# Kernel tuning notes

Measured on AMD Instinct MI355X. Metric: run time of the kernel, lower is better.

## Reference

```python
import jax, jax.numpy as jnp
import numpy as np

N_NODES = 100000
N_EDGES = 1600000
IN_DIM = 128
OUT_DIM = 64


def setup_inputs() -> dict:
    key = jax.random.key(0)
    k1, k2, k3, k4, k5, k6 = jax.random.split(key, 6)
    x = jax.random.normal(k1, (N_NODES, IN_DIM), dtype=jnp.float32)
    edge_row = jax.random.randint(k2, (N_EDGES,), 0, N_NODES, dtype=jnp.int32)
    edge_col = jax.random.randint(k3, (N_EDGES,), 0, N_NODES, dtype=jnp.int32)
    edge_val = jax.random.uniform(k4, (N_EDGES,), dtype=jnp.float32)
    W = jax.random.normal(k5, (IN_DIM, OUT_DIM), dtype=jnp.float32) * (1.0 / np.sqrt(IN_DIM))
    b = jax.random.normal(k6, (OUT_DIM,), dtype=jnp.float32) * 0.01
    return {"x": x, "edge_row": edge_row, "edge_col": edge_col,
            "edge_val": edge_val, "W": W, "b": b}


def reference(x, edge_row, edge_col, edge_val, W, b):
    # xw = Linear(x)  -> [N, OUT_DIM]
    xw = x @ W + b
    # SpMM: (A_hat @ xw)[r] = sum_e val[e] * xw[col[e]] for edges with row[e]==r
    msgs = edge_val[:, None] * xw[edge_col]          # [E, OUT_DIM]
    ax = jax.ops.segment_sum(msgs, edge_row, num_segments=N_NODES)  # [N, OUT_DIM]
    # ReLU; dropout p=0.0 is identity (eval mode)
    return jax.nn.relu(ax)
```

## Files before the change

### kernel.cpp

```cpp
#include <hip/hip_runtime.h>
#include <hip/hip_fp16.h>
#include <limits.h>

#define IN_DIM 128
#define OUT_DIM 64
#define NBUCK 782
#define RPB 128
#define CHUNK 4096
#define SCAP 4096


typedef _Float16 half8_t __attribute__((ext_vector_type(8)));
typedef float    f32x4  __attribute__((ext_vector_type(4)));

__device__ __forceinline__ int kmap(int g, int j) {
    return g * 4 + (j & 3) + 16 * (j >> 2);
}

__global__ __launch_bounds__(256) void prep_kernel(
    const float* __restrict__ W, __half* __restrict__ wf,
    int* __restrict__ bcount, int* __restrict__ cursor,
    int* __restrict__ row_ptr, int n_nodes, int n_edges) {
    const int t = threadIdx.x;
    for (int idx = t; idx < 4 * 4 * 64 * 8; idx += 256) {
        const int j    = idx & 7;
        const int lane = (idx >> 3) & 63;
        const int ks   = (idx >> 9) & 3;
        const int n    = idx >> 11;
        const int col  = n * 16 + (lane & 15);
        const int k    = ks * 32 + kmap(lane >> 4, j);
        wf[idx] = __float2half(W[k * OUT_DIM + col]);
    }
    if (bcount)
        for (int i = t; i < NBUCK; i += 256) { bcount[i] = 0; cursor[i] = 0; }
    if (row_ptr && t == 0) row_ptr[n_nodes] = n_edges;
}

__global__ __launch_bounds__(256) void gemm_hist_kernel(
    const float* __restrict__ x, const __half* __restrict__ wf,
    const float* __restrict__ b, __half* __restrict__ xw, int n_nodes,
    const int* __restrict__ erow, int* __restrict__ bcount, int n_edges) {
    __shared__ int h[NBUCK];
    const int t  = threadIdx.x;
    const int l  = t & 63;
    const int wv = t >> 6;
    const int g  = l >> 4;
    const int rowbase = blockIdx.x * 64 + wv * 16;
    const int row = rowbase + (l & 15);
    const bool rok = row < n_nodes;
    const float* xr = x + (size_t)row * IN_DIM;

    half8_t bf[4][4];
    const half8_t* wf8 = (const half8_t*)wf;
    #pragma unroll
    for (int n = 0; n < 4; ++n)
        #pragma unroll
        for (int ks = 0; ks < 4; ++ks)
            bf[n][ks] = wf8[(n * 4 + ks) * 64 + l];

    half8_t af[4];
    #pragma unroll
    for (int ks = 0; ks < 4; ++ks) {
        float4 c0 = rok ? *(const float4*)(xr + ks * 32 + g * 4)
                        : make_float4(0.f, 0.f, 0.f, 0.f);
        float4 c1 = rok ? *(const float4*)(xr + ks * 32 + 16 + g * 4)
                        : make_float4(0.f, 0.f, 0.f, 0.f);
        half8_t a;
        a[0] = (_Float16)c0.x; a[1] = (_Float16)c0.y;
        a[2] = (_Float16)c0.z; a[3] = (_Float16)c0.w;
        a[4] = (_Float16)c1.x; a[5] = (_Float16)c1.y;
        a[6] = (_Float16)c1.z; a[7] = (_Float16)c1.w;
        af[ks] = a;
    }

    f32x4 acc[4];
    #pragma unroll
    for (int n = 0; n < 4; ++n) acc[n] = (f32x4){0.f, 0.f, 0.f, 0.f};

    #pragma unroll
    for (int ks = 0; ks < 4; ++ks)
        #pragma unroll
        for (int n = 0; n < 4; ++n)
            acc[n] = __builtin_amdgcn_mfma_f32_16x16x32_f16(af[ks], bf[n][ks], acc[n], 0, 0, 0);

    float bias[4];
    #pragma unroll
    for (int n = 0; n < 4; ++n) bias[n] = b[n * 16 + (l & 15)];

    #pragma unroll
    for (int n = 0; n < 4; ++n)
        #pragma unroll
        for (int q = 0; q < 4; ++q) {
            const int ro = rowbase + g * 4 + q;
            if (ro < n_nodes)
                xw[(size_t)ro * OUT_DIM + n * 16 + (l & 15)] =
                    __float2half(acc[n][q] + bias[n]);
        }

    if (bcount && blockIdx.x < 512) {
        for (int i = t; i < NBUCK; i += 256) h[i] = 0;
        __syncthreads();
        const int stride = 512 * 256;
        for (int e = blockIdx.x * 256 + t; e < n_edges; e += stride)
            atomicAdd(&h[erow[e] >> 7], 1);
        __syncthreads();
        for (int i = t; i < NBUCK; i += 256)
            if (h[i]) atomicAdd(&bcount[i], h[i]);
    }
}

__global__ __launch_bounds__(512) void partition_kernel(
    const int* __restrict__ erow, const int* __restrict__ ecol,
    const float* __restrict__ eval_, const int* __restrict__ bcount,
    int* __restrict__ cursor, int2* __restrict__ ecs, int n_edges) {
    __shared__ int  hist[NBUCK];
    __shared__ int  lbase[NBUCK];
    __shared__ int  gdelta[NBUCK];
    __shared__ int  sbase[NBUCK];
    __shared__ int2 data[CHUNK];
    __shared__ int  gpos[CHUNK];
    __shared__ int  wsum[8];

    const int t = threadIdx.x;
    const int base = blockIdx.x * CHUNK;
    const int cnt = min(CHUNK, n_edges - base);

    for (int i = t; i < NBUCK; i += 512) hist[i] = 0;

    {
        const int i0 = 2 * t, i1 = 2 * t + 1;
        const int v0 = (i0 < NBUCK) ? bcount[i0] : 0;
        const int v1 = (i1 < NBUCK) ? bcount[i1] : 0;
        const int s2 = v0 + v1;
        int inc = s2;
        #pragma unroll
        for (int d = 1; d < 64; d <<= 1) {
            int u = __shfl_up(inc, d, 64);
            if ((t & 63) >= d) inc += u;
        }
        if ((t & 63) == 63) wsum[t >> 6] = inc;
        __syncthreads();
        int wp = 0;
        #pragma unroll
        for (int w = 0; w < 8; ++w) if (w < (t >> 6)) wp += wsum[w];
        const int ex = wp + (inc - s2);
        if (i0 < NBUCK) sbase[i0] = ex;
        if (i1 < NBUCK) sbase[i1] = ex + v0;
    }

    int   myrow[CHUNK / 512];
    int   mycol[CHUNK / 512];
    float myval[CHUNK / 512];
    #pragma unroll
    for (int i = 0; i < CHUNK / 512; ++i) {
        const int idx = t + i * 512;
        if (idx < cnt) {
            const int e = base + idx;
            myrow[i] = erow[e];
            mycol[i] = ecol[e];
            myval[i] = eval_[e];
            atomicAdd(&hist[myrow[i] >> 7], 1);
        }
    }
    __syncthreads();

    {
        const int i0 = 2 * t, i1 = 2 * t + 1;
        const int v0 = (i0 < NBUCK) ? hist[i0] : 0;
        const int v1 = (i1 < NBUCK) ? hist[i1] : 0;
        const int s2 = v0 + v1;
        int inc = s2;
        #pragma unroll
        for (int d = 1; d < 64; d <<= 1) {
            int u = __shfl_up(inc, d, 64);
            if ((t & 63) >= d) inc += u;
        }
        if ((t & 63) == 63) wsum[t >> 6] = inc;
        __syncthreads();
        int wp = 0;
        #pragma unroll
        for (int w = 0; w < 8; ++w) if (w < (t >> 6)) wp += wsum[w];
        const int ex = wp + (inc - s2);
        if (i0 < NBUCK) lbase[i0] = ex;
        if (i1 < NBUCK) lbase[i1] = ex + v0;
    }
    __syncthreads();

    for (int i = t; i < NBUCK; i += 512) {
        const int c = hist[i];
        gdelta[i] = c ? (sbase[i] + atomicAdd(&cursor[i], c) - lbase[i]) : 0;
    }
    __syncthreads();

    #pragma unroll
    for (int i = 0; i < CHUNK / 512; ++i) {
        const int idx = t + i * 512;
        if (idx < cnt) {
            const int bk = myrow[i] >> 7;
            const int slot = atomicAdd(&lbase[bk], 1);
            int2 p;
            p.x = (int)(((unsigned)(myrow[i] & (RPB - 1)) << 25) |
                        ((unsigned)mycol[i] << 7));
            p.y = __float_as_int(myval[i]);
            data[slot] = p;
            gpos[slot] = slot + gdelta[bk];
        }
    }
    __syncthreads();

    for (int slot = t; slot < cnt; slot += 512)
        ecs[gpos[slot]] = data[slot];
}

__global__ __launch_bounds__(512) void sort_kernel(
    const int* __restrict__ bcount, int2* __restrict__ ecs,
    int* __restrict__ row_ptr, int* __restrict__ bbase, int n_nodes) {
    __shared__ int2 data[SCAP];
    __shared__ int2 data2[SCAP];
    __shared__ int  hist[RPB];
    __shared__ int  sbase[NBUCK + 1];
    __shared__ int  wsum[8];
    __shared__ int  wtot;

    const int bk = blockIdx.x;
    const int t  = threadIdx.x;

    if (t < RPB) hist[t] = 0;

    {
        const int i0 = 2 * t, i1 = 2 * t + 1;
        const int v0 = (i0 < NBUCK) ? bcount[i0] : 0;
        const int v1 = (i1 < NBUCK) ? bcount[i1] : 0;
        const int s2 = v0 + v1;
        int inc = s2;
        #pragma unroll
        for (int d = 1; d < 64; d <<= 1) {
            int u = __shfl_up(inc, d, 64);
            if ((t & 63) >= d) inc += u;
        }
        if ((t & 63) == 63) wsum[t >> 6] = inc;
        __syncthreads();
        int wp = 0;
        #pragma unroll
        for (int w = 0; w < 8; ++w) if (w < (t >> 6)) wp += wsum[w];
        const int ex = wp + (inc - s2);
        if (i0 < NBUCK) sbase[i0] = ex;
        if (i1 < NBUCK) sbase[i1] = ex + v0;
        if (t == 511) sbase[NBUCK] = wp + inc;
    }
    __syncthreads();

    const int s   = sbase[bk];
    const int e   = sbase[bk + 1];
    const int cnt = e - s;
    const int rbase = bk * RPB;

    if (t == 0) {
        bbase[bk] = s;
        if (bk == NBUCK - 1) bbase[bk + 1] = e;
    }

    if (cnt > SCAP) {
        for (int r = t; r < RPB; r += 512)
            if (rbase + r < n_nodes) row_ptr[rbase + r] = INT_MIN;
        return;
    }

    for (int i = t; i < cnt; i += 512) {
        const int2 p = ecs[s + i];
        data[i] = p;
        atomicAdd(&hist[((unsigned)p.x) >> 25], 1);
    }
    __syncthreads();

    int inc = 0, v = 0;
    if (t < RPB) {
        v = hist[t];
        inc = v;
        #pragma unroll
        for (int d = 1; d < 64; d <<= 1) {
            int u = __shfl_up(inc, d, 64);
            if ((t & 63) >= d) inc += u;
        }
        if (t == 63) wtot = inc;
    }
    __syncthreads();
    if (t < RPB) {
        if (t >= 64) inc += wtot;
        const int ex = inc - v;
        if (rbase + t < n_nodes) row_ptr[rbase + t] = s + ex;
        hist[t] = ex;
    }
    __syncthreads();

    for (int i = t; i < cnt; i += 512) {
        const int2 p = data[i];
        const int pos = atomicAdd(&hist[((unsigned)p.x) >> 25], 1);
        data2[pos] = p;
    }
    __syncthreads();

    for (int i = t; i < cnt; i += 512) ecs[s + i] = data2[i];
}

__global__ __launch_bounds__(256) void gather_relu_kernel(
    const __half* __restrict__ xw, const int2* __restrict__ ecs,
    const int* __restrict__ row_ptr, const int* __restrict__ bbase,
    float* __restrict__ out, int n_nodes, int n_edges) {
    const int lane = threadIdx.x & 63;
    const int q    = lane & 7;
    const int g    = lane >> 3;
    const int wid  = (blockIdx.x * blockDim.x + threadIdx.x) >> 6;
    const int r0   = wid * 2;
    const int r1   = r0 + 1;
    if (r0 >= n_nodes) return;
    const bool has1 = (r1 < n_nodes);
    const char* xwb = (const char*)xw;

    const int s0raw = row_ptr[r0];
    const int s1raw = has1 ? row_ptr[r1] : INT_MIN;
    const bool ok0 = (s0raw != INT_MIN);
    const bool ok1 = has1 && (s1raw != INT_MIN);

    float acc0[8], acc1[8];
    #pragma unroll
    for (int i = 0; i < 8; ++i) { acc0[i] = 0.f; acc1[i] = 0.f; }

    if (ok0 && (ok1 || !has1)) {
        int e0;
        {
            const int n0 = row_ptr[r0 + 1];
            e0 = (n0 == INT_MIN) ? bbase[(r0 >> 7) + 1] : n0;
        }
        int e1 = 0, j1 = 0;
        if (ok1) {
            const int n1 = row_ptr[r1 + 1];
            e1 = (n1 == INT_MIN) ? bbase[(r1 >> 7) + 1] : n1;
            j1 = s1raw;
        }
        int j0 = s0raw;

        while (j0 < e0 || j1 < e1) {
            const bool a0 = j0 < e0;
            const bool a1 = j1 < e1;
            int2 p0, p1; float v0 = 0.f, v1 = 0.f;
            unsigned off0 = 0, off1 = 0;
            if (a0) {
                const int ei = j0 + g;
                p0 = ecs[min(ei, n_edges - 1)];
                v0 = (ei < e0) ? __int_as_float(p0.y) : 0.f;
                off0 = (((unsigned)p0.x) & 0x01FFFF80u) | ((unsigned)q << 4);
            }
            if (a1) {
                const int ei = j1 + g;
                p1 = ecs[min(ei, n_edges - 1)];
                v1 = (ei < e1) ? __int_as_float(p1.y) : 0.f;
                off1 = (((unsigned)p1.x) & 0x01FFFF80u) | ((unsigned)q << 4);
            }
            union { uint4 u; __half2 h[4]; } U0, U1;
            if (a0) U0.u = *(const uint4*)(xwb + off0);
            if (a1) U1.u = *(const uint4*)(xwb + off1);
            if (a0) {
                #pragma unroll
                for (int i = 0; i < 4; ++i) {
                    const float2 f = __half22float2(U0.h[i]);
                    acc0[2 * i]     = fmaf(v0, f.x, acc0[2 * i]);
                    acc0[2 * i + 1] = fmaf(v0, f.y, acc0[2 * i + 1]);
                }
                j0 += 8;
            }
            if (a1) {
                #pragma unroll
                for (int i = 0; i < 4; ++i) {
                    const float2 f = __half22float2(U1.h[i]);
                    acc1[2 * i]     = fmaf(v1, f.x, acc1[2 * i]);
                    acc1[2 * i + 1] = fmaf(v1, f.y, acc1[2 * i + 1]);
                }
                j1 += 8;
            }
        }
    } else {
        #pragma unroll 1
        for (int rr = 0; rr < 2; ++rr) {
            const int r = r0 + rr;
            if (r >= n_nodes) break;
            float* acc = rr ? acc1 : acc0;
            const int sr = row_ptr[r];
            if (sr != INT_MIN) {
                const int nr = row_ptr[r + 1];
                const int er = (nr == INT_MIN) ? bbase[(r >> 7) + 1] : nr;
                for (int j = sr; j < er; j += 8) {
                    const int ei = j + g;
                    const int2 p = ecs[min(ei, n_edges - 1)];
                    const float v = (ei < er) ? __int_as_float(p.y) : 0.f;
                    const unsigned off = (((unsigned)p.x) & 0x01FFFF80u) | ((unsigned)q << 4);
                    union { uint4 u; __half2 h[4]; } U;
                    U.u = *(const uint4*)(xwb + off);
                    #pragma unroll
                    for (int i = 0; i < 4; ++i) {
                        const float2 f = __half22float2(U.h[i]);
                        acc[2 * i]     = fmaf(v, f.x, acc[2 * i]);
                        acc[2 * i + 1] = fmaf(v, f.y, acc[2 * i + 1]);
                    }
                }
            } else {
                const int bk = r >> 7;
                const int bs = bbase[bk], be = bbase[bk + 1];
                const unsigned rl = (unsigned)(r & (RPB - 1));
                for (int j = bs; j < be; ++j) {
                    const int2 p = ecs[j];
                    if ((((unsigned)p.x) >> 25) == rl) {
                        const float v = __int_as_float(p.y);
                        const unsigned off = (((unsigned)p.x) & 0x01FFFF80u) | ((unsigned)q << 4);
                        union { uint4 u; __half2 h[4]; } U;
                        U.u = *(const uint4*)(xwb + off);
                        #pragma unroll
                        for (int i = 0; i < 4; ++i) {
                            const float2 f = __half22float2(U.h[i]);
                            acc[2 * i]     = fmaf(v * 0.125f, f.x, acc[2 * i]);
                            acc[2 * i + 1] = fmaf(v * 0.125f, f.y, acc[2 * i + 1]);
                        }
                    }
                }
            }
        }
    }

    #pragma unroll
    for (int d = 8; d < 64; d <<= 1) {
        #pragma unroll
        for (int i = 0; i < 8; ++i) {
            acc0[i] += __shfl_xor(acc0[i], d, 64);
            acc1[i] += __shfl_xor(acc1[i], d, 64);
        }
    }

    if (g == 0) {
        {
            float4 o0, o1;
            o0.x = fmaxf(acc0[0], 0.f); o0.y = fmaxf(acc0[1], 0.f);
            o0.z = fmaxf(acc0[2], 0.f); o0.w = fmaxf(acc0[3], 0.f);
            o1.x = fmaxf(acc0[4], 0.f); o1.y = fmaxf(acc0[5], 0.f);
            o1.z = fmaxf(acc0[6], 0.f); o1.w = fmaxf(acc0[7], 0.f);
            float* op = out + (size_t)r0 * OUT_DIM + q * 8;
            *(float4*)(op)     = o0;
            *(float4*)(op + 4) = o1;
        }
        if (has1) {
            float4 o0, o1;
            o0.x = fmaxf(acc1[0], 0.f); o0.y = fmaxf(acc1[1], 0.f);
            o0.z = fmaxf(acc1[2], 0.f); o0.w = fmaxf(acc1[3], 0.f);
            o1.x = fmaxf(acc1[4], 0.f); o1.y = fmaxf(acc1[5], 0.f);
            o1.z = fmaxf(acc1[6], 0.f); o1.w = fmaxf(acc1[7], 0.f);
            float* op = out + (size_t)r1 * OUT_DIM + q * 8;
            *(float4*)(op)     = o0;
            *(float4*)(op + 4) = o1;
        }
    }
}

__global__ __launch_bounds__(256) void edge_scatter_kernel(
    const __half* __restrict__ xw, const int* __restrict__ erow,
    const int* __restrict__ ecol, const float* __restrict__ eval_,
    float* __restrict__ out, int n_edges) {
    const int lane  = threadIdx.x & 63;
    const int wid   = (blockIdx.x * blockDim.x + threadIdx.x) >> 6;
    const int nwave = (gridDim.x * blockDim.x) >> 6;
    for (int e = wid; e < n_edges; e += nwave) {
        const float m = eval_[e] * __half2float(xw[(size_t)ecol[e] * OUT_DIM + lane]);
        atomicAdd(&out[(size_t)erow[e] * OUT_DIM + lane], m);
    }
}

__global__ __launch_bounds__(256) void relu_kernel(float4* __restrict__ p, int n4) {
    const int stride = gridDim.x * blockDim.x;
    for (int i = blockIdx.x * blockDim.x + threadIdx.x; i < n4; i += stride) {
        float4 v = p[i];
        v.x = fmaxf(v.x, 0.f); v.y = fmaxf(v.y, 0.f);
        v.z = fmaxf(v.z, 0.f); v.w = fmaxf(v.w, 0.f);
        p[i] = v;
    }
}

extern "C" void kernel_launch(void* const* d_in, const int* in_sizes, int n_in,
                              void* d_out, int out_size, void* d_ws, size_t ws_size,
                              hipStream_t stream) {
    const float* x     = (const float*)d_in[0];
    const int*   erow  = (const int*)d_in[1];
    const int*   ecol  = (const int*)d_in[2];
    const float* eval_ = (const float*)d_in[3];
    const float* W     = (const float*)d_in[4];
    const float* b     = (const float*)d_in[5];
    float*       out   = (float*)d_out;

    const int n_nodes = in_sizes[0] / IN_DIM;
    const int n_edges = in_sizes[1];

    auto align256 = [](size_t v) { return (v + 255) & ~(size_t)255; };
    size_t off_xw     = 0;
    size_t off_wf     = align256(off_xw     + (size_t)n_nodes * OUT_DIM * 2);
    size_t off_bcount = align256(off_wf     + (size_t)4 * 4 * 64 * 8 * 2);
    size_t off_cursor = align256(off_bcount + (size_t)NBUCK * 4);
    size_t off_bbase  = align256(off_cursor + (size_t)NBUCK * 4);
    size_t off_rowptr = align256(off_bbase  + (size_t)(NBUCK + 1) * 4);
    size_t off_ecs    = align256(off_rowptr + (size_t)(n_nodes + 1) * 4);
    size_t need       = off_ecs + (size_t)n_edges * 8;

    __half* xw = (__half*)((char*)d_ws + off_xw);
    __half* wf = (__half*)((char*)d_ws + off_wf);

    const bool main_path = (need <= ws_size) && (n_nodes <= NBUCK * RPB) && (n_edges > 0);

    if (main_path) {
        int*  bcount = (int*)((char*)d_ws + off_bcount);
        int*  cursor = (int*)((char*)d_ws + off_cursor);
        int*  bbase  = (int*)((char*)d_ws + off_bbase);
        int*  rowptr = (int*)((char*)d_ws + off_rowptr);
        int2* ecs    = (int2*)((char*)d_ws + off_ecs);

        prep_kernel<<<1, 256, 0, stream>>>(W, wf, bcount, cursor, rowptr, n_nodes, n_edges);
        gemm_hist_kernel<<<(n_nodes + 63) / 64, 256, 0, stream>>>(
            x, wf, b, xw, n_nodes, erow, bcount, n_edges);
        partition_kernel<<<(n_edges + CHUNK - 1) / CHUNK, 512, 0, stream>>>(
            erow, ecol, eval_, bcount, cursor, ecs, n_edges);
        sort_kernel<<<NBUCK, 512, 0, stream>>>(bcount, ecs, rowptr, bbase, n_nodes);
        gather_relu_kernel<<<(n_nodes + 7) / 8, 256, 0, stream>>>(
            xw, ecs, rowptr, bbase, out, n_nodes, n_edges);
    } else {
        prep_kernel<<<1, 256, 0, stream>>>(W, wf, nullptr, nullptr, nullptr, n_nodes, n_edges);
        gemm_hist_kernel<<<(n_nodes + 63) / 64, 256, 0, stream>>>(
            x, wf, b, xw, n_nodes, nullptr, nullptr, 0);
        hipMemsetAsync(d_out, 0, (size_t)out_size * sizeof(float), stream);
        edge_scatter_kernel<<<8192, 256, 0, stream>>>(xw, erow, ecol, eval_, out, n_edges);
        relu_kernel<<<2048, 256, 0, stream>>>((float4*)d_out, out_size / 4);
    }
}
```

Measured before the change: 112.3 us.

## Fuse per-bucket sort and gather-ReLU into one kernel using shared memory

```diff
diff --git a/kernel.cpp b/kernel.cpp
--- a/kernel.cpp
+++ b/kernel.cpp
@@ -19,8 +19,7 @@
 
 __global__ __launch_bounds__(256) void prep_kernel(
     const float* __restrict__ W, __half* __restrict__ wf,
-    int* __restrict__ bcount, int* __restrict__ cursor,
-    int* __restrict__ row_ptr, int n_nodes, int n_edges) {
+    int* __restrict__ bcount, int* __restrict__ cursor) {
     const int t = threadIdx.x;
     for (int idx = t; idx < 4 * 4 * 64 * 8; idx += 256) {
         const int j    = idx & 7;
@@ -33,7 +32,6 @@
     }
     if (bcount)
         for (int i = t; i < NBUCK; i += 256) { bcount[i] = 0; cursor[i] = 0; }
-    if (row_ptr && t == 0) row_ptr[n_nodes] = n_edges;
 }
 
 __global__ __launch_bounds__(256) void gemm_hist_kernel(
@@ -212,18 +210,23 @@
         ecs[gpos[slot]] = data[slot];
 }
 
-__global__ __launch_bounds__(512) void sort_kernel(
-    const int* __restrict__ bcount, int2* __restrict__ ecs,
-    int* __restrict__ row_ptr, int* __restrict__ bbase, int n_nodes) {
+__global__ __launch_bounds__(512) void bucket_gather_kernel(
+    const __half* __restrict__ xw, const int2* __restrict__ ecs,
+    const int* __restrict__ bcount, float* __restrict__ out,
+    int n_nodes, int n_edges) {
     __shared__ int2 data[SCAP];
-    __shared__ int2 data2[SCAP];
     __shared__ int  hist[RPB];
+    __shared__ int  rstart[RPB + 1];
     __shared__ int  sbase[NBUCK + 1];
     __shared__ int  wsum[8];
     __shared__ int  wtot;
 
-    const int bk = blockIdx.x;
-    const int t  = threadIdx.x;
+    const int bk   = blockIdx.x;
+    const int t    = threadIdx.x;
+    const int lane = t & 63;
+    const int wv   = t >> 6;
+    const int q    = lane & 7;
+    const int g    = lane >> 3;
 
     if (t < RPB) hist[t] = 0;
 
@@ -250,149 +253,144 @@
     }
     __syncthreads();
 
-    const int s   = sbase[bk];
-    const int e   = sbase[bk + 1];
-    const int cnt = e - s;
+    const int s     = sbase[bk];
+    const int e     = sbase[bk + 1];
+    const int cnt   = e - s;
     const int rbase = bk * RPB;
-
-    if (t == 0) {
-        bbase[bk] = s;
-        if (bk == NBUCK - 1) bbase[bk + 1] = e;
-    }
-
-    if (cnt > SCAP) {
-        for (int r = t; r < RPB; r += 512)
-            if (rbase + r < n_nodes) row_ptr[rbase + r] = INT_MIN;
-        return;
-    }
-
-    for (int i = t; i < cnt; i += 512) {
-        const int2 p = ecs[s + i];
-        data[i] = p;
-        atomicAdd(&hist[((unsigned)p.x) >> 25], 1);
-    }
-    __syncthreads();
-
-    int inc = 0, v = 0;
-    if (t < RPB) {
-        v = hist[t];
-        inc = v;
-        #pragma unroll
-        for (int d = 1; d < 64; d <<= 1) {
-            int u = __shfl_up(inc, d, 64);
-            if ((t & 63) >= d) inc += u;
-        }
-        if (t == 63) wtot = inc;
-    }
-    __syncthreads();
-    if (t < RPB) {
-        if (t >= 64) inc += wtot;
-        const int ex = inc - v;
-        if (rbase + t < n_nodes) row_ptr[rbase + t] = s + ex;
-        hist[t] = ex;
-    }
-    __syncthreads();
-
-    for (int i = t; i < cnt; i += 512) {
-        const int2 p = data[i];
-        const int pos = atomicAdd(&hist[((unsigned)p.x) >> 25], 1);
-        data2[pos] = p;
-    }
-    __syncthreads();
-
-    for (int i = t; i < cnt; i += 512) ecs[s + i] = data2[i];
-}
-
-__global__ __launch_bounds__(256) void gather_relu_kernel(
-    const __half* __restrict__ xw, const int2* __restrict__ ecs,
-    const int* __restrict__ row_ptr, const int* __restrict__ bbase,
-    float* __restrict__ out, int n_nodes, int n_edges) {
-    const int lane = threadIdx.x & 63;
-    const int q    = lane & 7;
-    const int g    = lane >> 3;
-    const int wid  = (blockIdx.x * blockDim.x + threadIdx.x) >> 6;
-    const int r0   = wid * 2;
-    const int r1   = r0 + 1;
-    if (r0 >= n_nodes) return;
-    const bool has1 = (r1 < n_nodes);
     const char* xwb = (const char*)xw;
 
-    const int s0raw = row_ptr[r0];
-    const int s1raw = has1 ? row_ptr[r1] : INT_MIN;
-    const bool ok0 = (s0raw != INT_MIN);
-    const bool ok1 = has1 && (s1raw != INT_MIN);
-
-    float acc0[8], acc1[8];
-    #pragma unroll
-    for (int i = 0; i < 8; ++i) { acc0[i] = 0.f; acc1[i] = 0.f; }
-
-    if (ok0 && (ok1 || !has1)) {
-        int e0;
+    if (cnt <= SCAP) {
+        for (int i = t; i < cnt; i += 512)
+            atomicAdd(&hist[((unsigned)ecs[s + i].x) >> 25], 1);
+        __syncthreads();
+
         {
-            const int n0 = row_ptr[r0 + 1];
-            e0 = (n0 == INT_MIN) ? bbase[(r0 >> 7) + 1] : n0;
-        }
-        int e1 = 0, j1 = 0;
-        if (ok1) {
-            const int n1 = row_ptr[r1 + 1];
-            e1 = (n1 == INT_MIN) ? bbase[(r1 >> 7) + 1] : n1;
-            j1 = s1raw;
-        }
-        int j0 = s0raw;
-
-        while (j0 < e0 || j1 < e1) {
-            const bool a0 = j0 < e0;
-            const bool a1 = j1 < e1;
-            int2 p0, p1; float v0 = 0.f, v1 = 0.f;
-            unsigned off0 = 0, off1 = 0;
-            if (a0) {
-                const int ei = j0 + g;
-                p0 = ecs[min(ei, n_edges - 1)];
-                v0 = (ei < e0) ? __int_as_float(p0.y) : 0.f;
-                off0 = (((unsigned)p0.x) & 0x01FFFF80u) | ((unsigned)q << 4);
-            }
-            if (a1) {
-                const int ei = j1 + g;
-                p1 = ecs[min(ei, n_edges - 1)];
-                v1 = (ei < e1) ? __int_as_float(p1.y) : 0.f;
-                off1 = (((unsigned)p1.x) & 0x01FFFF80u) | ((unsigned)q << 4);
-            }
-            union { uint4 u; __half2 h[4]; } U0, U1;
-            if (a0) U0.u = *(const uint4*)(xwb + off0);
-            if (a1) U1.u = *(const uint4*)(xwb + off1);
-            if (a0) {
+            int inc = 0, v = 0;
+            if (t < RPB) {
+                v = hist[t];
+                inc = v;
                 #pragma unroll
-                for (int i = 0; i < 4; ++i) {
-                    const float2 f = __half22float2(U0.h[i]);
-                    acc0[2 * i]     = fmaf(v0, f.x, acc0[2 * i]);
-                    acc0[2 * i + 1] = fmaf(v0, f.y, acc0[2 * i + 1]);
-                }
-                j0 += 8;
-            }
-            if (a1) {
+                for (int d = 1; d < 64; d <<= 1) {
+                    int u = __shfl_up(inc, d, 64);
+                    if ((t & 63) >= d) inc += u;
+                }
+                if (t == 63) wtot = inc;
+            }
+            __syncthreads();
+            if (t < RPB) {
+                if (t >= 64) inc += wtot;
+                rstart[t] = inc - v;
+                hist[t]   = inc - v;
+                if (t == RPB - 1) rstart[RPB] = inc;
+            }
+        }
+        __syncthreads();
+
+        for (int i = t; i < cnt; i += 512) {
+            const int2 p = ecs[s + i];
+            const int pos = atomicAdd(&hist[((unsigned)p.x) >> 25], 1);
+            data[pos] = p;
+        }
+        __syncthreads();
+
+        for (int rp = 0; rp < 8; ++rp) {
+            const int rl0 = wv * 16 + rp * 2;
+            const int rl1 = rl0 + 1;
+            int j0 = rstart[rl0];
+            const int e0 = rstart[rl0 + 1];
+            int j1 = rstart[rl1];
+            const int e1 = rstart[rl1 + 1];
+
+            float acc0[8], acc1[8];
+            #pragma unroll
+            for (int i = 0; i < 8; ++i) { acc0[i] = 0.f; acc1[i] = 0.f; }
+
+            while (j0 < e0 || j1 < e1) {
+                const bool a0 = j0 < e0;
+                const bool a1 = j1 < e1;
+                float v0 = 0.f, v1 = 0.f;
+                unsigned off0 = 0, off1 = 0;
+                if (a0) {
+                    const int ei = j0 + g;
+                    const int2 p = data[min(ei, cnt - 1)];
+                    v0 = (ei < e0) ? __int_as_float(p.y) : 0.f;
+                    off0 = (((unsigned)p.x) & 0x01FFFF80u) | ((unsigned)q << 4);
+                }
+                if (a1) {
+                    const int ei = j1 + g;
+                    const int2 p = data[min(ei, cnt - 1)];
+                    v1 = (ei < e1) ? __int_as_float(p.y) : 0.f;
+                    off1 = (((unsigned)p.x) & 0x01FFFF80u) | ((unsigned)q << 4);
+                }
+                union { uint4 u; __half2 h[4]; } U0, U1;
+                if (a0) U0.u = *(const uint4*)(xwb + off0);
+                if (a1) U1.u = *(const uint4*)(xwb + off1);
+                if (a0) {
+                    #pragma unroll
+                    for (int i = 0; i < 4; ++i) {
+                        const float2 f = __half22float2(U0.h[i]);
+                        acc0[2 * i]     = fmaf(v0, f.x, acc0[2 * i]);
+                        acc0[2 * i + 1] = fmaf(v0, f.y, acc0[2 * i + 1]);
+                    }
+                    j0 += 8;
+                }
+                if (a1) {
+                    #pragma unroll
+                    for (int i = 0; i < 4; ++i) {
+                        const float2 f = __half22float2(U1.h[i]);
+                        acc1[2 * i]     = fmaf(v1, f.x, acc1[2 * i]);
+                        acc1[2 * i + 1] = fmaf(v1, f.y, acc1[2 * i + 1]);
+                    }
+                    j1 += 8;
+                }
+            }
+
+            #pragma unroll
+            for (int d = 8; d < 64; d <<= 1) {
                 #pragma unroll
-                for (int i = 0; i < 4; ++i) {
-                    const float2 f = __half22float2(U1.h[i]);
-                    acc1[2 * i]     = fmaf(v1, f.x, acc1[2 * i]);
-                    acc1[2 * i + 1] = fmaf(v1, f.y, acc1[2 * i + 1]);
-                }
-                j1 += 8;
+                for (int i = 0; i < 8; ++i) {
+                    acc0[i] += __shfl_xor(acc0[i], d, 64);
+                    acc1[i] += __shfl_xor(acc1[i], d, 64);
+                }
+            }
+
+            if (g == 0) {
+                const int r0 = rbase + rl0;
+                const int r1 = rbase + rl1;
+                if (r0 < n_nodes) {
+                    float4 o0, o1;
+                    o0.x = fmaxf(acc0[0], 0.f); o0.y = fmaxf(acc0[1], 0.f);
+                    o0.z = fmaxf(acc0[2], 0.f); o0.w = fmaxf(acc0[3], 0.f);
+                    o1.x = fmaxf(acc0[4], 0.f); o1.y = fmaxf(acc0[5], 0.f);
+                    o1.z = fmaxf(acc0[6], 0.f); o1.w = fmaxf(acc0[7], 0.f);
+                    float* op = out + (size_t)r0 * OUT_DIM + q * 8;
+                    *(float4*)(op)     = o0;
+                    *(float4*)(op + 4) = o1;
+                }
+                if (r1 < n_nodes) {
+                    float4 o0, o1;
+                    o0.x = fmaxf(acc1[0], 0.f); o0.y = fmaxf(acc1[1], 0.f);
+                    o0.z = fmaxf(acc1[2], 0.f); o0.w = fmaxf(acc1[3], 0.f);
+                    o1.x = fmaxf(acc1[4], 0.f); o1.y = fmaxf(acc1[5], 0.f);
+                    o1.z = fmaxf(acc1[6], 0.f); o1.w = fmaxf(acc1[7], 0.f);
+                    float* op = out + (size_t)r1 * OUT_DIM + q * 8;
+                    *(float4*)(op)     = o0;
+                    *(float4*)(op + 4) = o1;
+                }
             }
         }
     } else {
-        #pragma unroll 1
-        for (int rr = 0; rr < 2; ++rr) {
-            const int r = r0 + rr;
+        for (int rr = 0; rr < 16; ++rr) {
+            const int r = rbase + wv * 16 + rr;
             if (r >= n_nodes) break;
-            float* acc = rr ? acc1 : acc0;
-            const int sr = row_ptr[r];
-            if (sr != INT_MIN) {
-                const int nr = row_ptr[r + 1];
-                const int er = (nr == INT_MIN) ? bbase[(r >> 7) + 1] : nr;
-                for (int j = sr; j < er; j += 8) {
-                    const int ei = j + g;
-                    const int2 p = ecs[min(ei, n_edges - 1)];
-                    const float v = (ei < er) ? __int_as_float(p.y) : 0.f;
+            float acc[8];
+            #pragma unroll
+            for (int i = 0; i < 8; ++i) acc[i] = 0.f;
+            const unsigned rl = (unsigned)(r & (RPB - 1));
+            for (int j = s + g; j < e; j += 8) {
+                const int2 p = ecs[j];
+                if ((((unsigned)p.x) >> 25) == rl) {
+                    const float v = __int_as_float(p.y);
                     const unsigned off = (((unsigned)p.x) & 0x01FFFF80u) | ((unsigned)q << 4);
                     union { uint4 u; __half2 h[4]; } U;
                     U.u = *(const uint4*)(xwb + off);
@@ -403,58 +401,22 @@
                         acc[2 * i + 1] = fmaf(v, f.y, acc[2 * i + 1]);
                     }
                 }
-            } else {
-                const int bk = r >> 7;
-                const int bs = bbase[bk], be = bbase[bk + 1];
-                const unsigned rl = (unsigned)(r & (RPB - 1));
-                for (int j = bs; j < be; ++j) {
-                    const int2 p = ecs[j];
-                    if ((((unsigned)p.x) >> 25) == rl) {
-                        const float v = __int_as_float(p.y);
-                        const unsigned off = (((unsigned)p.x) & 0x01FFFF80u) | ((unsigned)q << 4);
-                        union { uint4 u; __half2 h[4]; } U;
-                        U.u = *(const uint4*)(xwb + off);
-                        #pragma unroll
-                        for (int i = 0; i < 4; ++i) {
-                            const float2 f = __half22float2(U.h[i]);
-                            acc[2 * i]     = fmaf(v * 0.125f, f.x, acc[2 * i]);
-                            acc[2 * i + 1] = fmaf(v * 0.125f, f.y, acc[2 * i + 1]);
-                        }
-                    }
-                }
-            }
-        }
-    }
-
-    #pragma unroll
-    for (int d = 8; d < 64; d <<= 1) {
-        #pragma unroll
-        for (int i = 0; i < 8; ++i) {
-            acc0[i] += __shfl_xor(acc0[i], d, 64);
-            acc1[i] += __shfl_xor(acc1[i], d, 64);
-        }
-    }
-
-    if (g == 0) {
-        {
-            float4 o0, o1;
-            o0.x = fmaxf(acc0[0], 0.f); o0.y = fmaxf(acc0[1], 0.f);
-            o0.z = fmaxf(acc0[2], 0.f); o0.w = fmaxf(acc0[3], 0.f);
-            o1.x = fmaxf(acc0[4], 0.f); o1.y = fmaxf(acc0[5], 0.f);
-            o1.z = fmaxf(acc0[6], 0.f); o1.w = fmaxf(acc0[7], 0.f);
-            float* op = out + (size_t)r0 * OUT_DIM + q * 8;
-            *(float4*)(op)     = o0;
-            *(float4*)(op + 4) = o1;
-        }
-        if (has1) {
-            float4 o0, o1;
-            o0.x = fmaxf(acc1[0], 0.f); o0.y = fmaxf(acc1[1], 0.f);
-            o0.z = fmaxf(acc1[2], 0.f); o0.w = fmaxf(acc1[3], 0.f);
-            o1.x = fmaxf(acc1[4], 0.f); o1.y = fmaxf(acc1[5], 0.f);
-            o1.z = fmaxf(acc1[6], 0.f); o1.w = fmaxf(acc1[7], 0.f);
-            float* op = out + (size_t)r1 * OUT_DIM + q * 8;
-            *(float4*)(op)     = o0;
-            *(float4*)(op + 4) = o1;
+            }
+            #pragma unroll
+            for (int d = 8; d < 64; d <<= 1)
+                #pragma unroll
+                for (int i = 0; i < 8; ++i)
+                    acc[i] += __shfl_xor(acc[i], d, 64);
+            if (g == 0) {
+                float4 o0, o1;
+                o0.x = fmaxf(acc[0], 0.f); o0.y = fmaxf(acc[1], 0.f);
+                o0.z = fmaxf(acc[2], 0.f); o0.w = fmaxf(acc[3], 0.f);
+                o1.x = fmaxf(acc[4], 0.f); o1.y = fmaxf(acc[5], 0.f);
+                o1.z = fmaxf(acc[6], 0.f); o1.w = fmaxf(acc[7], 0.f);
+                float* op = out + (size_t)r * OUT_DIM + q * 8;
+                *(float4*)(op)     = o0;
+                *(float4*)(op + 4) = o1;
+            }
         }
     }
 }
@@ -501,9 +463,7 @@
     size_t off_wf     = align256(off_xw     + (size_t)n_nodes * OUT_DIM * 2);
     size_t off_bcount = align256(off_wf     + (size_t)4 * 4 * 64 * 8 * 2);
     size_t off_cursor = align256(off_bcount + (size_t)NBUCK * 4);
-    size_t off_bbase  = align256(off_cursor + (size_t)NBUCK * 4);
-    size_t off_rowptr = align256(off_bbase  + (size_t)(NBUCK + 1) * 4);
-    size_t off_ecs    = align256(off_rowptr + (size_t)(n_nodes + 1) * 4);
+    size_t off_ecs    = align256(off_cursor + (size_t)NBUCK * 4);
     size_t need       = off_ecs + (size_t)n_edges * 8;
 
     __half* xw = (__half*)((char*)d_ws + off_xw);
@@ -514,20 +474,17 @@
     if (main_path) {
         int*  bcount = (int*)((char*)d_ws + off_bcount);
         int*  cursor = (int*)((char*)d_ws + off_cursor);
-        int*  bbase  = (int*)((char*)d_ws + off_bbase);
-        int*  rowptr = (int*)((char*)d_ws + off_rowptr);
         int2* ecs    = (int2*)((char*)d_ws + off_ecs);
 
-        prep_kernel<<<1, 256, 0, stream>>>(W, wf, bcount, cursor, rowptr, n_nodes, n_edges);
+        prep_kernel<<<1, 256, 0, stream>>>(W, wf, bcount, cursor);
         gemm_hist_kernel<<<(n_nodes + 63) / 64, 256, 0, stream>>>(
             x, wf, b, xw, n_nodes, erow, bcount, n_edges);
         partition_kernel<<<(n_edges + CHUNK - 1) / CHUNK, 512, 0, stream>>>(
             erow, ecol, eval_, bcount, cursor, ecs, n_edges);
-        sort_kernel<<<NBUCK, 512, 0, stream>>>(bcount, ecs, rowptr, bbase, n_nodes);
-        gather_relu_kernel<<<(n_nodes + 7) / 8, 256, 0, stream>>>(
-            xw, ecs, rowptr, bbase, out, n_nodes, n_edges);
+        bucket_gather_kernel<<<NBUCK, 512, 0, stream>>>(
+            xw, ecs, bcount, out, n_nodes, n_edges);
     } else {
-        prep_kernel<<<1, 256, 0, stream>>>(W, wf, nullptr, nullptr, nullptr, n_nodes, n_edges);
+        prep_kernel<<<1, 256, 0, stream>>>(W, wf, nullptr, nullptr);
         gemm_hist_kernel<<<(n_nodes + 63) / 64, 256, 0, stream>>>(
             x, wf, b, xw, n_nodes, nullptr, nullptr, 0);
         hipMemsetAsync(d_out, 0, (size_t)out_size * sizeof(float), stream);
```

Measured after the change: 106.1 us. 1.06x faster.
